# Performance work log

Measured on AMD Instinct MI355X. Metric: run time of the kernel, lower is better.

## Reference

```python
import jax, jax.numpy as jnp
import numpy as np

D_MODEL = 256
D_INNER = 512   # expand_factor * d_model
D_STATE = 64
DT_RANK = 4     # ceil(d_model / 64)
D_CONV = 4
B = 8
L = 144


def setup_inputs() -> dict:
    key = jax.random.key(0)
    ks = jax.random.split(key, 8)
    s = lambda k, shp, sc=0.02: jax.random.normal(k, shp, jnp.float32) * sc
    x = jax.random.normal(ks[0], (B, L, D_MODEL), jnp.float32)
    lastin = jnp.zeros((B, D_INNER, D_STATE), jnp.float32)  # accepted but unused by the scan
    W_in = s(ks[1], (2 * D_INNER, D_MODEL))              # in_proj (no bias)
    conv_w = s(ks[2], (D_INNER, 1, D_CONV), 0.1)          # depthwise conv kernel [O, I/groups, K]
    conv_b = jnp.zeros((D_INNER,), jnp.float32)
    W_x = s(ks[3], (DT_RANK + 2 * D_STATE, D_INNER))      # x_proj (no bias)
    W_dt = s(ks[4], (D_INNER, DT_RANK), 0.1)
    b_dt = jnp.full((D_INNER,), -4.0, jnp.float32)        # softplus -> small dt, like mamba init
    A_log = jnp.log(jnp.tile(jnp.arange(1, D_STATE + 1, dtype=jnp.float32), (D_INNER, 1)))
    Dp = jnp.ones((D_INNER,), jnp.float32)
    W_out = s(ks[5], (D_MODEL, D_INNER))                  # out_proj (no bias)
    return dict(x=x, lastin=lastin, W_in=W_in, conv_w=conv_w, conv_b=conv_b,
                W_x=W_x, W_dt=W_dt, b_dt=b_dt, A_log=A_log, Dp=Dp, W_out=W_out)


def _forward(x, lastin, W_in, conv_w, conv_b, W_x, W_dt, b_dt, A_log, Dp, W_out):
    # in_proj and split
    xz = jnp.einsum('bld,ed->ble', x, W_in)               # [B, L, 2*d_inner]
    ix, z = jnp.split(xz, 2, axis=-1)

    # depthwise causal-ish conv1d: torch padding=2 then slice [:L] == padding (2, 1)
    ix = jnp.swapaxes(ix, 1, 2)                            # [B, d_inner, L]
    ix = jax.lax.conv_general_dilated(
        ix, conv_w, window_strides=(1,), padding=[(2, 1)],
        feature_group_count=D_INNER, dimension_numbers=('NCH', 'OIH', 'NCH'))
    ix = ix + conv_b[None, :, None]
    ix = jnp.swapaxes(ix, 1, 2)                            # [B, L, d_inner]
    ix = jax.nn.silu(ix)

    # ssm parameterization
    A = -jnp.exp(A_log)                                    # [d_inner, d_state]
    dBC = jnp.einsum('bld,ed->ble', ix, W_x)               # [B, L, dt_rank + 2*d_state]
    dt_r = dBC[..., :DT_RANK]
    Bm = dBC[..., DT_RANK:DT_RANK + D_STATE]               # [B, L, d_state]
    Cm = dBC[..., DT_RANK + D_STATE:]                      # [B, L, d_state]
    delta = jax.nn.softplus(jnp.einsum('blr,dr->bld', dt_r, W_dt) + b_dt)  # [B, L, d_inner]

    # discretization
    deltaA = jnp.exp(delta[..., None] * A)                 # [B, L, d_inner, d_state]
    BX = (delta * ix)[..., None] * Bm[:, :, None, :]       # [B, L, d_inner, d_state]

    # sequential selective scan: h_t = deltaA_t * h_{t-1} + BX_t
    def step(h, inp):
        dA_t, bx_t = inp
        h = dA_t * h + bx_t
        return h, h

    h0 = jnp.zeros((x.shape[0], D_INNER, D_STATE), x.dtype)
    _, hs = jax.lax.scan(step, h0, (jnp.moveaxis(deltaA, 1, 0), jnp.moveaxis(BX, 1, 0)))
    # hs: [L, B, d_inner, d_state]

    y = jnp.einsum('lbdn,lbn->bld', hs, jnp.moveaxis(Cm, 1, 0))  # [B, L, d_inner]
    y = y + Dp * ix

    out = jnp.einsum('bld,ed->ble', y * jax.nn.silu(z), W_out)   # [B, L, d_model]
    return out


def reference(x, lastin, W_in, conv_w, conv_b, W_x, W_dt, b_dt, A_log, Dp, W_out):
    return _forward(x, lastin, W_in, conv_w, conv_b, W_x, W_dt, b_dt, A_log, Dp, W_out)
```

## Files before the change

kernel.cpp:

```cpp
#include <hip/hip_runtime.h>

#define B_SZ 8
#define L_SEQ 144
#define NTOK 1152
#define D_MODEL 256
#define D_INNER 512
#define D_STATE 64
#define DT_RANK 4
#define NDBC 132
#define SLAB 152064

typedef __attribute__((ext_vector_type(8))) short bf16x8;
typedef __attribute__((ext_vector_type(4))) float f32x4;

__device__ __forceinline__ void cvt8(const float4& f0, const float4& f1,
                                     int4& hi, int4& lo) {
    const float f[8] = {f0.x, f0.y, f0.z, f0.w, f1.x, f1.y, f1.z, f1.w};
    unsigned h[8], l[8];
#pragma unroll
    for (int e = 0; e < 8; ++e) {
        const unsigned u = __float_as_uint(f[e]);
        const unsigned t = u + 0x7FFFu + ((u >> 16) & 1u);
        h[e] = t >> 16;
        l[e] = __float_as_uint(f[e] - __uint_as_float(t & 0xFFFF0000u)) >> 16;
    }
    hi = make_int4((int)(h[0] | (h[1] << 16)), (int)(h[2] | (h[3] << 16)),
                   (int)(h[4] | (h[5] << 16)), (int)(h[6] | (h[7] << 16)));
    lo = make_int4((int)(l[0] | (l[1] << 16)), (int)(l[2] | (l[3] << 16)),
                   (int)(l[4] | (l[5] << 16)), (int)(l[6] | (l[7] << 16)));
}

__device__ __forceinline__ void unpack8(const int4& p0, const int4& p1,
                                        bf16x8& hv, bf16x8& lv) {
    const unsigned u[8] = {(unsigned)p0.x, (unsigned)p0.y, (unsigned)p0.z,
                           (unsigned)p0.w, (unsigned)p1.x, (unsigned)p1.y,
                           (unsigned)p1.z, (unsigned)p1.w};
    int h[4], l[4];
#pragma unroll
    for (int i = 0; i < 4; ++i) {
        h[i] = (int)((u[2 * i] >> 16) | (u[2 * i + 1] & 0xFFFF0000u));
        l[i] = (int)((u[2 * i] & 0xFFFFu) | (u[2 * i + 1] << 16));
    }
    hv = *(bf16x8*)h;
    lv = *(bf16x8*)l;
}

__device__ __forceinline__ int bc_perm(const int p) {
    return (p < DT_RANK) ? p
         : (((p - DT_RANK) & 1) ? (DT_RANK + D_STATE + ((p - DT_RANK) >> 1))
                                : (DT_RANK + ((p - DT_RANK) >> 1)));
}

#define LW 40
__global__ __launch_bounds__(256) void gemm1_mfma(const float* __restrict__ W_in,
                                                  const float* __restrict__ x,
                                                  float* __restrict__ xz) {
    __shared__ unsigned short Ah[64][LW], Al[64][LW], Bh[64][LW], Bl[64][LW];
    const int tid = threadIdx.x;
    const int m0 = blockIdx.y * 64, n0 = blockIdx.x * 64;
    const int r = tid >> 2, kq = (tid & 3) * 8;
    const int w = tid >> 6, lane = tid & 63;
    const int wm = (w & 1) * 32, wn = (w >> 1) * 32;
    const int fr = lane & 15, fk = (lane >> 4) * 8;
    f32x4 acc[2][2] = {};
    float4 a0, a1, b0, b1;

    auto loadG = [&](const int k0) {
        const float* ap = W_in + (size_t)(m0 + r) * D_MODEL + k0 + kq;
        const float* bp = x    + (size_t)(n0 + r) * D_MODEL + k0 + kq;
        a0 = *(const float4*)ap; a1 = *(const float4*)(ap + 4);
        b0 = *(const float4*)bp; b1 = *(const float4*)(bp + 4);
    };

    loadG(0);
    for (int k0 = 0; k0 < D_MODEL; k0 += 32) {
        int4 hi, lo;
        __syncthreads();
        cvt8(a0, a1, hi, lo);
        *(int4*)&Ah[r][kq] = hi; *(int4*)&Al[r][kq] = lo;
        cvt8(b0, b1, hi, lo);
        *(int4*)&Bh[r][kq] = hi; *(int4*)&Bl[r][kq] = lo;
        __syncthreads();
        if (k0 + 32 < D_MODEL) loadG(k0 + 32);
        bf16x8 ah[2], al[2], bh[2], bl[2];
#pragma unroll
        for (int i = 0; i < 2; ++i) {
            ah[i] = *(const bf16x8*)&Ah[wm + 16 * i + fr][fk];
            al[i] = *(const bf16x8*)&Al[wm + 16 * i + fr][fk];
            bh[i] = *(const bf16x8*)&Bh[wn + 16 * i + fr][fk];
            bl[i] = *(const bf16x8*)&Bl[wn + 16 * i + fr][fk];
        }
#pragma unroll
        for (int i = 0; i < 2; ++i)
#pragma unroll
            for (int j = 0; j < 2; ++j) {
                acc[i][j] = __builtin_amdgcn_mfma_f32_16x16x32_bf16(ah[i], bh[j], acc[i][j], 0, 0, 0);
                acc[i][j] = __builtin_amdgcn_mfma_f32_16x16x32_bf16(ah[i], bl[j], acc[i][j], 0, 0, 0);
                acc[i][j] = __builtin_amdgcn_mfma_f32_16x16x32_bf16(al[i], bh[j], acc[i][j], 0, 0, 0);
            }
    }
    const int orow = (lane >> 4) * 4;
#pragma unroll
    for (int i = 0; i < 2; ++i)
#pragma unroll
        for (int j = 0; j < 2; ++j)
#pragma unroll
            for (int q = 0; q < 4; ++q)
                xz[(size_t)(m0 + wm + 16 * i + orow + q) * NTOK
                   + n0 + wn + 16 * j + fr] = acc[i][j][q];
}

__global__ __launch_bounds__(256) void gemm2_mfma(const float* __restrict__ xz,
                                                  const float* __restrict__ W_x,
                                                  float* __restrict__ slab,
                                                  const float* __restrict__ cw,
                                                  const float* __restrict__ cb) {
    __shared__ unsigned short Ah[64][LW], Al[64][LW], Bh[64][LW], Bl[64][LW];
    const int tid = threadIdx.x;
    const int n0 = blockIdx.x * 64;
    const int m0 = blockIdx.y * 64;
    const int kbeg = blockIdx.z * 64;
    const int ar = tid >> 3, ac8 = (tid & 7) * 8;
    const int br = tid >> 2, bq8 = (tid & 3) * 8;
    const int brow = bc_perm(n0 + br);
    const int w = tid >> 6, lane = tid & 63;
    const int wm = (w & 1) * 32, wn = (w >> 1) * 32;
    const int fr = lane & 15, fk = (lane >> 4) * 8;
    const int t = (m0 + ac8) % L_SEQ;
    f32x4 acc[2][2] = {};
    slab += (size_t)blockIdx.z * SLAB;

#pragma unroll
    for (int ks = 0; ks < 2; ++ks) {
        const int k0 = kbeg + ks * 32;
        const int d = k0 + ar;
        const float* row = xz + (size_t)d * NTOK + m0 + ac8;
        const float4 a0 = *(const float4*)row;
        const float4 a1 = *(const float4*)(row + 4);
        const float xm2 = (t > 0) ? row[-2] : 0.f;
        const float xm1 = (t > 0) ? row[-1] : 0.f;
        const float xp8 = (t < L_SEQ - 8) ? row[8] : 0.f;
        const float4 cw4 = *(const float4*)(cw + d * 4);
        const float cbv = cb[d];
        float4 bv0 = make_float4(0.f, 0.f, 0.f, 0.f), bv1 = bv0;
        if (n0 + br < NDBC) {
            const float* bp = W_x + (size_t)brow * D_INNER + k0 + bq8;
            bv0 = *(const float4*)bp; bv1 = *(const float4*)(bp + 4);
        }
        __syncthreads();
        {
            const float in[11] = {xm2, xm1, a0.x, a0.y, a0.z, a0.w,
                                  a1.x, a1.y, a1.z, a1.w, xp8};
#pragma unroll
            for (int j = 0; j < 8; ++j) {
                float s = cbv;
                s = fmaf(cw4.x, in[j + 0], s);
                s = fmaf(cw4.y, in[j + 1], s);
                s = fmaf(cw4.z, in[j + 2], s);
                s = fmaf(cw4.w, in[j + 3], s);
                const float g = s * __builtin_amdgcn_rcpf(1.f + __expf(-s));
                const unsigned u = __float_as_uint(g);
                const unsigned tt = u + 0x7FFFu + ((u >> 16) & 1u);
                Ah[ac8 + j][ar] = (unsigned short)(tt >> 16);
                Al[ac8 + j][ar] = (unsigned short)(__float_as_uint(
                                     g - __uint_as_float(tt & 0xFFFF0000u)) >> 16);
            }
            int4 hi, lo;
            cvt8(bv0, bv1, hi, lo);
            *(int4*)&Bh[br][bq8] = hi; *(int4*)&Bl[br][bq8] = lo;
        }
        __syncthreads();
        bf16x8 ah[2], al[2], bh[2], bl[2];
#pragma unroll
        for (int i = 0; i < 2; ++i) {
            ah[i] = *(const bf16x8*)&Ah[wm + 16 * i + fr][fk];
            al[i] = *(const bf16x8*)&Al[wm + 16 * i + fr][fk];
            bh[i] = *(const bf16x8*)&Bh[wn + 16 * i + fr][fk];
            bl[i] = *(const bf16x8*)&Bl[wn + 16 * i + fr][fk];
        }
#pragma unroll
        for (int i = 0; i < 2; ++i)
#pragma unroll
            for (int j = 0; j < 2; ++j) {
                acc[i][j] = __builtin_amdgcn_mfma_f32_16x16x32_bf16(ah[i], bh[j], acc[i][j], 0, 0, 0);
                acc[i][j] = __builtin_amdgcn_mfma_f32_16x16x32_bf16(ah[i], bl[j], acc[i][j], 0, 0, 0);
                acc[i][j] = __builtin_amdgcn_mfma_f32_16x16x32_bf16(al[i], bh[j], acc[i][j], 0, 0, 0);
            }
    }
    const int orow = (lane >> 4) * 4;
#pragma unroll
    for (int i = 0; i < 2; ++i)
#pragma unroll
        for (int j = 0; j < 2; ++j) {
            const int gn = n0 + wn + 16 * j + fr;
            if (gn < NDBC)
#pragma unroll
                for (int q = 0; q < 4; ++q)
                    slab[(size_t)(m0 + wm + 16 * i + orow + q) * NDBC + gn]
                        = acc[i][j][q];
        }
}

__global__ __launch_bounds__(256) void gemm3_mfma(const unsigned* __restrict__ gpk,
                                                  const float* __restrict__ W_out,
                                                  float* __restrict__ out) {
    __shared__ float red[4][16][64];
    const int tid = threadIdx.x;
    const int n0 = blockIdx.x * 64, m0 = blockIdx.y * 16;
    const int w = tid >> 6, lane = tid & 63;
    const int kw = w * 128;
    const int fr = lane & 15, fk = (lane >> 4) * 8;
    f32x4 acc[4] = {};
#pragma unroll
    for (int m = 0; m < 4; ++m) {
        const int k0 = kw + m * 32;
        bf16x8 ah, al, bh[4], bl[4];
        const unsigned* ap = gpk + (size_t)(m0 + fr) * D_INNER + k0 + fk;
        unpack8(*(const int4*)ap, *(const int4*)(ap + 4), ah, al);
#pragma unroll
        for (int j = 0; j < 4; ++j) {
            const float* bp = W_out + (size_t)(n0 + 16 * j + fr) * D_INNER + k0 + fk;
            int4 hi, lo;
            cvt8(*(const float4*)bp, *(const float4*)(bp + 4), hi, lo);
            bh[j] = *(bf16x8*)&hi;
            bl[j] = *(bf16x8*)&lo;
        }
#pragma unroll
        for (int j = 0; j < 4; ++j) {
            acc[j] = __builtin_amdgcn_mfma_f32_16x16x32_bf16(ah, bh[j], acc[j], 0, 0, 0);
            acc[j] = __builtin_amdgcn_mfma_f32_16x16x32_bf16(ah, bl[j], acc[j], 0, 0, 0);
            acc[j] = __builtin_amdgcn_mfma_f32_16x16x32_bf16(al, bh[j], acc[j], 0, 0, 0);
        }
    }
    const int orow = (lane >> 4) * 4;
#pragma unroll
    for (int j = 0; j < 4; ++j)
#pragma unroll
        for (int q = 0; q < 4; ++q)
            red[w][orow + q][16 * j + fr] = acc[j][q];
    __syncthreads();
    const int row = tid >> 4, col = (tid & 15) * 4;
    const float4 s0 = *(const float4*)&red[0][row][col];
    const float4 s1 = *(const float4*)&red[1][row][col];
    const float4 s2 = *(const float4*)&red[2][row][col];
    const float4 s3 = *(const float4*)&red[3][row][col];
    *(float4*)(out + (size_t)(m0 + row) * D_MODEL + n0 + col) = make_float4(
        s0.x + s1.x + s2.x + s3.x, s0.y + s1.y + s2.y + s3.y,
        s0.z + s1.z + s2.z + s3.z, s0.w + s1.w + s2.w + s3.w);
}

__global__ __launch_bounds__(256) void reduce8_k(const float4* __restrict__ in,
                                                 float4* __restrict__ out,
                                                 const int n4, const int s4) {
    const int i = blockIdx.x * 256 + threadIdx.x;
    if (i >= n4) return;
    float4 a = in[i];
#pragma unroll
    for (int s = 1; s < 8; ++s) {
        const float4 b = in[i + s * s4];
        a.x += b.x; a.y += b.y; a.z += b.z; a.w += b.w;
    }
    out[i] = a;
}

__device__ __forceinline__ float bcast(const float v, const int i) {
    return __int_as_float(__builtin_amdgcn_readlane(__float_as_int(v), i));
}

template<int CNT>
__device__ __forceinline__ void scan_chunk(const float* __restrict__ dBC,
                                           const float* __restrict__ xz,
                                           unsigned* __restrict__ gpk,
                                           float (*__restrict__ Pw)[65],
                                           const int d, const int base, const int t0,
                                           const float An2, const float4 wdt,
                                           const float bdt, const float dpv,
                                           const float4 cw4, const float cbv,
                                           const int lane, float& h) {
    float delta_r = 0.f, dix_r = 0.f, dpix_r = 0.f, sz_r = 0.f;
    if (lane < CNT) {
        const int t = t0 + lane;
        const int tok = base + t;
        const float* row = xz + (size_t)d * NTOK + tok;
        float s0 = cbv;
        if (t >= 2) s0 = fmaf(cw4.x, row[-2], s0);
        if (t >= 1) s0 = fmaf(cw4.y, row[-1], s0);
        s0 = fmaf(cw4.z, row[0], s0);
        if (t < L_SEQ - 1) s0 = fmaf(cw4.w, row[1], s0);
        const float ixv = s0 * __builtin_amdgcn_rcpf(1.f + __expf(-s0));

        const float4 dt4 = *(const float4*)(dBC + (size_t)tok * NDBC);
        float s = fmaf(dt4.x, wdt.x, bdt);
        s = fmaf(dt4.y, wdt.y, s);
        s = fmaf(dt4.z, wdt.z, s);
        s = fmaf(dt4.w, wdt.w, s);
        const float delta = fmaxf(s, 0.f) + __logf(1.f + __expf(-fabsf(s)));
        const float zv = xz[(size_t)(D_INNER + d) * NTOK + tok];
        delta_r = delta;
        dix_r   = delta * ixv;
        dpix_r  = dpv * ixv;
        sz_r    = zv * __builtin_amdgcn_rcpf(1.f + __expf(-zv));
    }
#pragma unroll
    for (int i = 0; i < CNT; ++i) {
        const float2 bc = *(const float2*)(dBC + (size_t)(base + t0 + i) * NDBC
                                           + DT_RANK + 2 * lane);
        const float dlt = bcast(delta_r, i);
        const float dxv = bcast(dix_r, i);
        const float dA = __builtin_amdgcn_exp2f(dlt * An2);
        h = fmaf(dA, h, dxv * bc.x);
        Pw[i][lane] = h * bc.y;
    }
    const int tl = lane & 31, hf = lane >> 5;
    float s2 = 0.f;
    if (tl < CNT) {
#pragma unroll
        for (int j = 0; j < 32; ++j) s2 += Pw[tl][hf * 32 + j];
    }
    s2 += __shfl_xor(s2, 32, 64);
    if (hf == 0 && tl < CNT) {
        const float g = (s2 + dpix_r) * sz_r;
        const unsigned u = __float_as_uint(g);
        const unsigned t = u + 0x7FFFu + ((u >> 16) & 1u);
        const unsigned lo16 = __float_as_uint(
            g - __uint_as_float(t & 0xFFFF0000u)) >> 16;
        gpk[(size_t)(base + t0 + tl) * D_INNER + d] = (t & 0xFFFF0000u) | lo16;
    }
}

__global__ __launch_bounds__(256) void scan_k(const float* __restrict__ dBC,
                                              const float* __restrict__ xz,
                                              const float* __restrict__ W_dt,
                                              const float* __restrict__ b_dt,
                                              const float* __restrict__ A_log,
                                              const float* __restrict__ Dp,
                                              const float* __restrict__ conv_w,
                                              const float* __restrict__ conv_b,
                                              unsigned* __restrict__ gpk) {
    __shared__ float P[4][32][65];
    const int w = threadIdx.x >> 6, lane = threadIdx.x & 63;
    const int b = blockIdx.x >> 7, dg = blockIdx.x & 127;
    const int d = (dg << 2) | w;
    const int base = b * L_SEQ;
    const float An2 = -__expf(A_log[(d << 6) + lane]) * 1.44269504088896f;
    const float4 wdt = *(const float4*)(W_dt + (d << 2));
    const float bdt = b_dt[d], dpv = Dp[d];
    const float4 cw4 = *(const float4*)(conv_w + (d << 2));
    const float cbv = conv_b[d];
    float h = 0.f;
    scan_chunk<32>(dBC, xz, gpk, P[w], d, base, 0,   An2, wdt, bdt, dpv, cw4, cbv, lane, h);
    scan_chunk<32>(dBC, xz, gpk, P[w], d, base, 32,  An2, wdt, bdt, dpv, cw4, cbv, lane, h);
    scan_chunk<32>(dBC, xz, gpk, P[w], d, base, 64,  An2, wdt, bdt, dpv, cw4, cbv, lane, h);
    scan_chunk<32>(dBC, xz, gpk, P[w], d, base, 96,  An2, wdt, bdt, dpv, cw4, cbv, lane, h);
    scan_chunk<16>(dBC, xz, gpk, P[w], d, base, 128, An2, wdt, bdt, dpv, cw4, cbv, lane, h);
}

extern "C" void kernel_launch(void* const* d_in, const int* in_sizes, int n_in,
                              void* d_out, int out_size, void* d_ws, size_t ws_size,
                              hipStream_t stream) {
    const float* x      = (const float*)d_in[0];
    const float* W_in   = (const float*)d_in[2];
    const float* conv_w = (const float*)d_in[3];
    const float* conv_b = (const float*)d_in[4];
    const float* W_x    = (const float*)d_in[5];
    const float* W_dt   = (const float*)d_in[6];
    const float* b_dt   = (const float*)d_in[7];
    const float* A_log  = (const float*)d_in[8];
    const float* Dp     = (const float*)d_in[9];
    const float* W_out  = (const float*)d_in[10];
    float* out = (float*)d_out;

    float* ws  = (float*)d_ws;
    float* xz  = ws;
    float* dBC = xz + 1179648;
    float* sl3 = dBC + 152064;
    unsigned* gpk = (unsigned*)(sl3 + 8 * SLAB);

    gemm1_mfma<<<dim3(18, 16), 256, 0, stream>>>(W_in, x, xz);
    gemm2_mfma<<<dim3(3, 18, 8), 256, 0, stream>>>(xz, W_x, sl3, conv_w, conv_b);
    reduce8_k<<<dim3(149), 256, 0, stream>>>((const float4*)sl3, (float4*)dBC,
                                             NTOK * NDBC / 4, NTOK * NDBC / 4);
    scan_k<<<dim3(B_SZ * 128), 256, 0, stream>>>(dBC, xz, W_dt, b_dt, A_log, Dp,
                                                 conv_w, conv_b, gpk);
    gemm3_mfma<<<dim3(4, 72), 256, 0, stream>>>(gpk, W_out, out);
}
```

Before: 129.9 us.

## Replace split-K gemm2 with in-block K reduction and drop reduce kernel

The x_proj GEMM used to split K across 8 grid slices, write partial slabs to global memory and sum them in a separate reduce8_k launch. It now follows the gemm3 pattern: each block owns a 16-token by 64-column tile, its four waves each cover a quarter of K, and the partials are summed through shared memory before one direct store to dBC. Operands are loaded straight into registers without LDS staging, and the conv plus SiLU is recomputed per element. This removes one kernel launch and the partial-slab traffic, at the cost of fewer blocks (216 instead of 432) and scattered, uncoalesced per-lane reads of xz and W_x.

```diff
diff --git a/kernel.cpp b/kernel.cpp
--- a/kernel.cpp
+++ b/kernel.cpp
@@ -8,7 +8,6 @@
 #define D_STATE 64
 #define DT_RANK 4
 #define NDBC 132
-#define SLAB 152064
 
 typedef __attribute__((ext_vector_type(8))) short bf16x8;
 typedef __attribute__((ext_vector_type(4))) float f32x4;
@@ -112,93 +111,77 @@
 
 __global__ __launch_bounds__(256) void gemm2_mfma(const float* __restrict__ xz,
                                                   const float* __restrict__ W_x,
-                                                  float* __restrict__ slab,
+                                                  float* __restrict__ dBC,
                                                   const float* __restrict__ cw,
                                                   const float* __restrict__ cb) {
-    __shared__ unsigned short Ah[64][LW], Al[64][LW], Bh[64][LW], Bl[64][LW];
+    __shared__ float red[4][16][64];
     const int tid = threadIdx.x;
-    const int n0 = blockIdx.x * 64;
-    const int m0 = blockIdx.y * 64;
-    const int kbeg = blockIdx.z * 64;
-    const int ar = tid >> 3, ac8 = (tid & 7) * 8;
-    const int br = tid >> 2, bq8 = (tid & 3) * 8;
-    const int brow = bc_perm(n0 + br);
+    const int n0 = blockIdx.x * 64, m0 = blockIdx.y * 16;
     const int w = tid >> 6, lane = tid & 63;
-    const int wm = (w & 1) * 32, wn = (w >> 1) * 32;
+    const int kw = w * 128;
     const int fr = lane & 15, fk = (lane >> 4) * 8;
-    const int t = (m0 + ac8) % L_SEQ;
-    f32x4 acc[2][2] = {};
-    slab += (size_t)blockIdx.z * SLAB;
-
-#pragma unroll
-    for (int ks = 0; ks < 2; ++ks) {
-        const int k0 = kbeg + ks * 32;
-        const int d = k0 + ar;
-        const float* row = xz + (size_t)d * NTOK + m0 + ac8;
-        const float4 a0 = *(const float4*)row;
-        const float4 a1 = *(const float4*)(row + 4);
-        const float xm2 = (t > 0) ? row[-2] : 0.f;
-        const float xm1 = (t > 0) ? row[-1] : 0.f;
-        const float xp8 = (t < L_SEQ - 8) ? row[8] : 0.f;
-        const float4 cw4 = *(const float4*)(cw + d * 4);
-        const float cbv = cb[d];
-        float4 bv0 = make_float4(0.f, 0.f, 0.f, 0.f), bv1 = bv0;
-        if (n0 + br < NDBC) {
-            const float* bp = W_x + (size_t)brow * D_INNER + k0 + bq8;
-            bv0 = *(const float4*)bp; bv1 = *(const float4*)(bp + 4);
-        }
-        __syncthreads();
-        {
-            const float in[11] = {xm2, xm1, a0.x, a0.y, a0.z, a0.w,
-                                  a1.x, a1.y, a1.z, a1.w, xp8};
-#pragma unroll
-            for (int j = 0; j < 8; ++j) {
-                float s = cbv;
-                s = fmaf(cw4.x, in[j + 0], s);
-                s = fmaf(cw4.y, in[j + 1], s);
-                s = fmaf(cw4.z, in[j + 2], s);
-                s = fmaf(cw4.w, in[j + 3], s);
-                const float g = s * __builtin_amdgcn_rcpf(1.f + __expf(-s));
-                const unsigned u = __float_as_uint(g);
-                const unsigned tt = u + 0x7FFFu + ((u >> 16) & 1u);
-                Ah[ac8 + j][ar] = (unsigned short)(tt >> 16);
-                Al[ac8 + j][ar] = (unsigned short)(__float_as_uint(
-                                     g - __uint_as_float(tt & 0xFFFF0000u)) >> 16);
+    const int tok = m0 + fr;
+    const int t = tok % L_SEQ;
+    f32x4 acc[4] = {};
+#pragma unroll
+    for (int m = 0; m < 4; ++m) {
+        const int k0 = kw + m * 32;
+        float g8[8];
+#pragma unroll
+        for (int e = 0; e < 8; ++e) {
+            const int d = k0 + fk + e;
+            const float* row = xz + (size_t)d * NTOK + tok;
+            const float4 cw4 = *(const float4*)(cw + d * 4);
+            float s = cb[d];
+            if (t >= 2) s = fmaf(cw4.x, row[-2], s);
+            if (t >= 1) s = fmaf(cw4.y, row[-1], s);
+            s = fmaf(cw4.z, row[0], s);
+            if (t < L_SEQ - 1) s = fmaf(cw4.w, row[1], s);
+            g8[e] = s * __builtin_amdgcn_rcpf(1.f + __expf(-s));
+        }
+        int4 ahi, alo;
+        cvt8(make_float4(g8[0], g8[1], g8[2], g8[3]),
+             make_float4(g8[4], g8[5], g8[6], g8[7]), ahi, alo);
+        const bf16x8 ah = *(bf16x8*)&ahi, al = *(bf16x8*)&alo;
+        bf16x8 bh[4], bl[4];
+#pragma unroll
+        for (int j = 0; j < 4; ++j) {
+            const int n = n0 + 16 * j + fr;
+            float4 b0 = make_float4(0.f, 0.f, 0.f, 0.f), b1 = b0;
+            if (n < NDBC) {
+                const float* bp = W_x + (size_t)bc_perm(n) * D_INNER + k0 + fk;
+                b0 = *(const float4*)bp; b1 = *(const float4*)(bp + 4);
             }
             int4 hi, lo;
-            cvt8(bv0, bv1, hi, lo);
-            *(int4*)&Bh[br][bq8] = hi; *(int4*)&Bl[br][bq8] = lo;
-        }
-        __syncthreads();
-        bf16x8 ah[2], al[2], bh[2], bl[2];
-#pragma unroll
-        for (int i = 0; i < 2; ++i) {
-            ah[i] = *(const bf16x8*)&Ah[wm + 16 * i + fr][fk];
-            al[i] = *(const bf16x8*)&Al[wm + 16 * i + fr][fk];
-            bh[i] = *(const bf16x8*)&Bh[wn + 16 * i + fr][fk];
-            bl[i] = *(const bf16x8*)&Bl[wn + 16 * i + fr][fk];
-        }
-#pragma unroll
-        for (int i = 0; i < 2; ++i)
-#pragma unroll
-            for (int j = 0; j < 2; ++j) {
-                acc[i][j] = __builtin_amdgcn_mfma_f32_16x16x32_bf16(ah[i], bh[j], acc[i][j], 0, 0, 0);
-                acc[i][j] = __builtin_amdgcn_mfma_f32_16x16x32_bf16(ah[i], bl[j], acc[i][j], 0, 0, 0);
-                acc[i][j] = __builtin_amdgcn_mfma_f32_16x16x32_bf16(al[i], bh[j], acc[i][j], 0, 0, 0);
-            }
+            cvt8(b0, b1, hi, lo);
+            bh[j] = *(bf16x8*)&hi;
+            bl[j] = *(bf16x8*)&lo;
+        }
+#pragma unroll
+        for (int j = 0; j < 4; ++j) {
+            acc[j] = __builtin_amdgcn_mfma_f32_16x16x32_bf16(ah, bh[j], acc[j], 0, 0, 0);
+            acc[j] = __builtin_amdgcn_mfma_f32_16x16x32_bf16(ah, bl[j], acc[j], 0, 0, 0);
+            acc[j] = __builtin_amdgcn_mfma_f32_16x16x32_bf16(al, bh[j], acc[j], 0, 0, 0);
+        }
     }
     const int orow = (lane >> 4) * 4;
 #pragma unroll
-    for (int i = 0; i < 2; ++i)
-#pragma unroll
-        for (int j = 0; j < 2; ++j) {
-            const int gn = n0 + wn + 16 * j + fr;
-            if (gn < NDBC)
-#pragma unroll
-                for (int q = 0; q < 4; ++q)
-                    slab[(size_t)(m0 + wm + 16 * i + orow + q) * NDBC + gn]
-                        = acc[i][j][q];
-        }
+    for (int j = 0; j < 4; ++j)
+#pragma unroll
+        for (int q = 0; q < 4; ++q)
+            red[w][orow + q][16 * j + fr] = acc[j][q];
+    __syncthreads();
+    const int row = tid >> 4, col = (tid & 15) * 4;
+    const int gn = n0 + col;
+    if (gn < NDBC) {
+        const float4 s0 = *(const float4*)&red[0][row][col];
+        const float4 s1 = *(const float4*)&red[1][row][col];
+        const float4 s2 = *(const float4*)&red[2][row][col];
+        const float4 s3 = *(const float4*)&red[3][row][col];
+        *(float4*)(dBC + (size_t)(m0 + row) * NDBC + gn) = make_float4(
+            s0.x + s1.x + s2.x + s3.x, s0.y + s1.y + s2.y + s3.y,
+            s0.z + s1.z + s2.z + s3.z, s0.w + s1.w + s2.w + s3.w);
+    }
 }
 
 __global__ __launch_bounds__(256) void gemm3_mfma(const unsigned* __restrict__ gpk,
@@ -247,20 +230,6 @@
     *(float4*)(out + (size_t)(m0 + row) * D_MODEL + n0 + col) = make_float4(
         s0.x + s1.x + s2.x + s3.x, s0.y + s1.y + s2.y + s3.y,
         s0.z + s1.z + s2.z + s3.z, s0.w + s1.w + s2.w + s3.w);
-}
-
-__global__ __launch_bounds__(256) void reduce8_k(const float4* __restrict__ in,
-                                                 float4* __restrict__ out,
-                                                 const int n4, const int s4) {
-    const int i = blockIdx.x * 256 + threadIdx.x;
-    if (i >= n4) return;
-    float4 a = in[i];
-#pragma unroll
-    for (int s = 1; s < 8; ++s) {
-        const float4 b = in[i + s * s4];
-        a.x += b.x; a.y += b.y; a.z += b.z; a.w += b.w;
-    }
-    out[i] = a;
 }
 
 __device__ __forceinline__ float bcast(const float v, const int i) {
@@ -373,13 +342,10 @@
     float* ws  = (float*)d_ws;
     float* xz  = ws;
     float* dBC = xz + 1179648;
-    float* sl3 = dBC + 152064;
-    unsigned* gpk = (unsigned*)(sl3 + 8 * SLAB);
+    unsigned* gpk = (unsigned*)(dBC + 152064);
 
     gemm1_mfma<<<dim3(18, 16), 256, 0, stream>>>(W_in, x, xz);
-    gemm2_mfma<<<dim3(3, 18, 8), 256, 0, stream>>>(xz, W_x, sl3, conv_w, conv_b);
-    reduce8_k<<<dim3(149), 256, 0, stream>>>((const float4*)sl3, (float4*)dBC,
-                                             NTOK * NDBC / 4, NTOK * NDBC / 4);
+    gemm2_mfma<<<dim3(3, 72), 256, 0, stream>>>(xz, W_x, dBC, conv_w, conv_b);
     scan_k<<<dim3(B_SZ * 128), 256, 0, stream>>>(dBC, xz, W_dt, b_dt, A_log, Dp,
                                                  conv_w, conv_b, gpk);
     gemm3_mfma<<<dim3(4, 72), 256, 0, stream>>>(gpk, W_out, out);
```

After: 155.8 us. 20.0% more time.
